# Kernel optimization log

Hardware: AMD Instinct MI355X
Metric: run time of the kernel (lower is better)

Reference implementation:

```python
import jax, jax.numpy as jnp
import numpy as np
import math


def _neighbor_stack(x):
    # x: [b, nc, w, d] -> [b, nc, 3, w, d] with zero-padded prev/next chunks
    prev = jnp.pad(x[:, :-1], ((0, 0), (1, 0), (0, 0), (0, 0)))
    nxt = jnp.pad(x[:, 1:], ((0, 0), (0, 1), (0, 0), (0, 0)))
    return jnp.stack([prev, x, nxt], axis=2)


def local_attention(q, kv, Wq, Wkv, Wo, w):
    b, L, d_model = q.shape
    d_head = Wkv.shape[1] // 2
    h = d_model // d_head
    nc = L // w

    qp = (q @ Wq).reshape(b, L, h, d_head) / math.sqrt(d_head)
    kvp = kv @ Wkv  # [b, L, 2*d_head], single shared KV head (MQA)
    k, v = kvp[..., :d_head], kvp[..., d_head:]

    cq = qp.reshape(b, nc, w, h, d_head)
    k3 = _neighbor_stack(k.reshape(b, nc, w, d_head))  # [b, nc, 3, w, d]
    v3 = _neighbor_stack(v.reshape(b, nc, w, d_head))  # [b, nc, 3, w, d]

    # scores over (prev, self, next) chunks; padded edge chunks contribute
    # zero scores (exp(0)=1 in softmax), exactly as the torch F.pad(value=0) does.
    scores = jnp.einsum('bcxhd,bcpyd->bcxhpy', cq, k3)  # [b,nc,w,h,3,w]
    probs = jax.nn.softmax(scores.reshape(b, nc, w, h, 3 * w), axis=-1)
    probs = probs.reshape(b, nc, w, h, 3, w)

    ctx = jnp.einsum('bcxhpy,bcpyd->bcxhd', probs, v3)  # [b,nc,w,h,d]
    ctx = ctx.reshape(b, L, d_model)
    return ctx @ Wo


def setup_inputs() -> dict:
    key = jax.random.key(0)
    k1, k2, k3, k4, k5 = jax.random.split(key, 5)
    b, L, d_model, n_head = 1, 4096, 1024, 16
    d_head = d_model // n_head
    scale = 0.02
    return {
        'q': jax.random.normal(k1, (b, L, d_model), dtype=jnp.float32),
        'kv': jax.random.normal(k2, (b, L, d_model), dtype=jnp.float32),
        'Wq': jax.random.normal(k3, (d_model, d_model), dtype=jnp.float32) * scale,
        'Wkv': jax.random.normal(k4, (d_model, 2 * d_head), dtype=jnp.float32) * scale,
        'Wo': jax.random.normal(k5, (d_model, d_model), dtype=jnp.float32) * scale,
        'w': 512,
    }


def reference(q, kv, Wq, Wkv, Wo, w):
    return local_attention(q, kv, Wq, Wkv, Wo, w)
```

## Files before the change

kernel.cpp:

```cpp
#include <hip/hip_runtime.h>
#include <hip/hip_bf16.h>

typedef unsigned short u16;
typedef unsigned int u32;
typedef __attribute__((ext_vector_type(8))) short bf16x8;
typedef __attribute__((ext_vector_type(4))) float f32x4;
typedef __attribute__((ext_vector_type(16))) float f32x16;
typedef __attribute__((ext_vector_type(4))) u32 u32x4;

__device__ __forceinline__ u16 f2bf(float x) {
  __hip_bfloat16 h = __float2bfloat16(x);
  return __builtin_bit_cast(u16, h);
}

__device__ __forceinline__ u32 cvtpk(float lo, float hi) {
  u32 d;
  asm("v_cvt_pk_bf16_f32 %0, %1, %2" : "=v"(d) : "v"(lo), "v"(hi));
  return d;
}

#if __has_builtin(__builtin_amdgcn_exp2f)
#define EXP2(x) __builtin_amdgcn_exp2f(x)
#else
#define EXP2(x) __expf((x) * 0.6931471805599453f)
#endif

__device__ __forceinline__ bf16x8 mk_frag(u32 a, u32 b, u32 c, u32 d) {
  u32x4 v = {a, b, c, d};
  return __builtin_bit_cast(bf16x8, v);
}

__device__ __forceinline__ f32x16 mfma32(bf16x8 a, bf16x8 b, f32x16 c) {
  return __builtin_amdgcn_mfma_f32_32x32x16_bf16(a, b, c, 0, 0, 0);
}

__device__ __forceinline__ void gload16(const void* g, void* lds) {
  __builtin_amdgcn_global_load_lds((const __attribute__((address_space(1))) void*)g,
                                   (__attribute__((address_space(3))) void*)lds, 16, 0, 0);
}

__global__ __launch_bounds__(256) void cvt_tw(const float* __restrict__ q, const float* __restrict__ kv,
                                              const float* __restrict__ Wq, const float* __restrict__ Wkv,
                                              const float* __restrict__ Wo, u16* __restrict__ qkbf,
                                              u16* __restrict__ wqt, u16* __restrict__ wkvt,
                                              u16* __restrict__ wot) {
  __shared__ float T[64][65];
  const int t = threadIdx.x;
  const int bid = blockIdx.x;
  if (bid < 4096) {
    int idx = bid * 256 + t;
    const float* src = (idx < 524288) ? q : kv;
    int li = idx & 524287;
    const float4* p = (const float4*)src + (size_t)li * 2;
    float4 a = p[0], b = p[1];
    bf16x8 vv;
    vv[0] = (short)f2bf(a.x); vv[1] = (short)f2bf(a.y);
    vv[2] = (short)f2bf(a.z); vv[3] = (short)f2bf(a.w);
    vv[4] = (short)f2bf(b.x); vv[5] = (short)f2bf(b.y);
    vv[6] = (short)f2bf(b.z); vv[7] = (short)f2bf(b.w);
    *(bf16x8*)(qkbf + (size_t)idx * 8) = vv;
    return;
  }
  const int wb = bid - 4096;
  const float* W; u16* Wt; int N, bx, by;
  if (wb < 256)      { W = Wq;  Wt = wqt;  N = 1024; bx = wb & 15; by = wb >> 4; }
  else if (wb < 512) { int b = wb - 256; W = Wo;  Wt = wot;  N = 1024; bx = b & 15; by = b >> 4; }
  else               { int b = wb - 512; W = Wkv; Wt = wkvt; N = 128;  bx = b & 1;  by = b >> 1; }
  const int K = 1024;
  const int n0 = bx * 64, k0 = by * 64;
  #pragma unroll
  for (int pass = 0; pass < 4; ++pass) {
    int r = pass * 16 + (t >> 4);
    int c = (t & 15) * 4;
    float4 v = *(const float4*)(W + (size_t)(k0 + r) * N + n0 + c);
    T[r][c] = v.x; T[r][c + 1] = v.y; T[r][c + 2] = v.z; T[r][c + 3] = v.w;
  }
  __syncthreads();
  #pragma unroll
  for (int s = 0; s < 2; ++s) {
    int n = s * 32 + (t >> 3);
    int kk = (t & 7) * 8;
    bf16x8 vv;
    #pragma unroll
    for (int i = 0; i < 8; ++i) vv[i] = (short)f2bf(T[kk + i][n]);
    *(bf16x8*)(Wt + (size_t)(n0 + n) * K + k0 + kk) = vv;
  }
}

template<int BF16OUT>
__global__ __launch_bounds__(256, 3) void gemm_bt(const u16* __restrict__ A, const u16* __restrict__ Bt,
                                                  void* __restrict__ Cout, int N, int K, float scale) {
  __shared__ __attribute__((aligned(16))) u16 As[128 * 128];
  __shared__ __attribute__((aligned(16))) u16 Bs[64 * 128];
  const int t = threadIdx.x;
  const int lane = t & 63, wv = t >> 6;
  const int g = lane >> 4, i16 = lane & 15;
  const int m0 = blockIdx.y * 128, n0 = blockIdx.x * 64;
  const int wr = wv >> 1, wc = wv & 1;
  f32x4 acc[4][2] = {};
  for (int kt = 0; kt < K; kt += 128) {
    #pragma unroll
    for (int j = 0; j < 8; ++j) {
      int p = j * 4096 + t * 16;
      int row = p >> 8;
      int lg = (p & 255) ^ ((row & 15) << 4);
      gload16(A + (size_t)(m0 + row) * K + kt + (lg >> 1), (char*)As + p);
    }
    #pragma unroll
    for (int j = 0; j < 4; ++j) {
      int p = j * 4096 + t * 16;
      int row = p >> 8;
      int lg = (p & 255) ^ ((row & 15) << 4);
      gload16(Bt + (size_t)(n0 + row) * K + kt + (lg >> 1), (char*)Bs + p);
    }
    __syncthreads();
    bf16x8 af[4][4], bfr[4][2];
    #pragma unroll
    for (int kf = 0; kf < 4; ++kf) {
      #pragma unroll
      for (int x = 0; x < 4; ++x) {
        int ra = wr * 64 + x * 16 + i16;
        af[kf][x] = *(const bf16x8*)((const char*)As + ((ra * 256 + kf * 64 + g * 16) ^ ((ra & 15) << 4)));
      }
      #pragma unroll
      for (int x = 0; x < 2; ++x) {
        int rb = wc * 32 + x * 16 + i16;
        bfr[kf][x] = *(const bf16x8*)((const char*)Bs + ((rb * 256 + kf * 64 + g * 16) ^ ((rb & 15) << 4)));
      }
    }
    #pragma unroll
    for (int kf = 0; kf < 4; ++kf)
      #pragma unroll
      for (int mi = 0; mi < 4; ++mi)
        #pragma unroll
        for (int ni = 0; ni < 2; ++ni)
          acc[mi][ni] = __builtin_amdgcn_mfma_f32_16x16x32_bf16(af[kf][mi], bfr[kf][ni], acc[mi][ni], 0, 0, 0);
    __syncthreads();
  }
  #pragma unroll
  for (int mi = 0; mi < 4; ++mi)
    #pragma unroll
    for (int ni = 0; ni < 2; ++ni)
      #pragma unroll
      for (int r = 0; r < 4; ++r) {
        size_t off = (size_t)(m0 + wr * 64 + mi * 16 + g * 4 + r) * N + (n0 + wc * 32 + ni * 16 + i16);
        float v = acc[mi][ni][r] * scale;
        if (BF16OUT) ((u16*)Cout)[off] = f2bf(v);
        else ((float*)Cout)[off] = v;
      }
}

__global__ __launch_bounds__(256, 3) void gemm_qkv(const u16* __restrict__ qbf, const u16* __restrict__ kvbf,
                                                   const u16* __restrict__ wqt, const u16* __restrict__ wkvt,
                                                   u16* __restrict__ qp, u16* __restrict__ kvp,
                                                   u16* __restrict__ vtg) {
  __shared__ __attribute__((aligned(16))) u16 As[128 * 128];
  __shared__ __attribute__((aligned(16))) u16 Bs[64 * 128];
  const int t = threadIdx.x;
  const int lane = t & 63, wv = t >> 6;
  const int g = lane >> 4, i16 = lane & 15;
  const int wr = wv >> 1, wc = wv & 1;
  const int K = 1024;
  const int bid = blockIdx.x;
  const bool iskv = bid >= 512;
  const u16* A; const u16* Bt; int m0, n0;
  if (!iskv) { A = qbf;  Bt = wqt;  m0 = (bid >> 4) * 128; n0 = (bid & 15) * 64; }
  else       { int b = bid - 512; A = kvbf; Bt = wkvt; m0 = (b >> 1) * 128; n0 = (b & 1) * 64; }
  f32x4 acc[4][2] = {};
  for (int kt = 0; kt < K; kt += 128) {
    #pragma unroll
    for (int j = 0; j < 8; ++j) {
      int p = j * 4096 + t * 16;
      int row = p >> 8;
      int lg = (p & 255) ^ ((row & 15) << 4);
      gload16(A + (size_t)(m0 + row) * K + kt + (lg >> 1), (char*)As + p);
    }
    #pragma unroll
    for (int j = 0; j < 4; ++j) {
      int p = j * 4096 + t * 16;
      int row = p >> 8;
      int lg = (p & 255) ^ ((row & 15) << 4);
      gload16(Bt + (size_t)(n0 + row) * K + kt + (lg >> 1), (char*)Bs + p);
    }
    __syncthreads();
    bf16x8 af[4][4], bfr[4][2];
    #pragma unroll
    for (int kf = 0; kf < 4; ++kf) {
      #pragma unroll
      for (int x = 0; x < 4; ++x) {
        int ra = wr * 64 + x * 16 + i16;
        af[kf][x] = *(const bf16x8*)((const char*)As + ((ra * 256 + kf * 64 + g * 16) ^ ((ra & 15) << 4)));
      }
      #pragma unroll
      for (int x = 0; x < 2; ++x) {
        int rb = wc * 32 + x * 16 + i16;
        bfr[kf][x] = *(const bf16x8*)((const char*)Bs + ((rb * 256 + kf * 64 + g * 16) ^ ((rb & 15) << 4)));
      }
    }
    #pragma unroll
    for (int kf = 0; kf < 4; ++kf)
      #pragma unroll
      for (int mi = 0; mi < 4; ++mi)
        #pragma unroll
        for (int ni = 0; ni < 2; ++ni)
          acc[mi][ni] = __builtin_amdgcn_mfma_f32_16x16x32_bf16(af[kf][mi], bfr[kf][ni], acc[mi][ni], 0, 0, 0);
    __syncthreads();
  }
  if (!iskv) {
    #pragma unroll
    for (int mi = 0; mi < 4; ++mi)
      #pragma unroll
      for (int ni = 0; ni < 2; ++ni)
        #pragma unroll
        for (int r = 0; r < 4; ++r)
          qp[(size_t)(m0 + wr * 64 + mi * 16 + g * 4 + r) * 1024 + n0 + wc * 32 + ni * 16 + i16] =
              f2bf(acc[mi][ni][r] * 0.18033688011112042f);
  } else if (n0 == 0) {
    #pragma unroll
    for (int mi = 0; mi < 4; ++mi)
      #pragma unroll
      for (int ni = 0; ni < 2; ++ni)
        #pragma unroll
        for (int r = 0; r < 4; ++r)
          kvp[(size_t)(m0 + wr * 64 + mi * 16 + g * 4 + r) * 64 + wc * 32 + ni * 16 + i16] =
              f2bf(acc[mi][ni][r]);
  } else {
    u16* CT = (u16*)As;
    #pragma unroll
    for (int mi = 0; mi < 4; ++mi)
      #pragma unroll
      for (int ni = 0; ni < 2; ++ni)
        #pragma unroll
        for (int r = 0; r < 4; ++r)
          CT[(wc * 32 + ni * 16 + i16) * 128 + wr * 64 + mi * 16 + g * 4 + r] = f2bf(acc[mi][ni][r]);
    __syncthreads();
    int d = t >> 2, c4 = t & 3;
    const u16* src = CT + d * 128 + c4 * 32;
    u16* dst = vtg + (size_t)d * 4096 + m0 + c4 * 32;
    #pragma unroll
    for (int j = 0; j < 4; ++j)
      *(bf16x8*)(dst + j * 8) = *(const bf16x8*)(src + j * 8);
  }
}

__global__ __launch_bounds__(256, 2) void attn_kernel(const u16* __restrict__ qp, const u16* __restrict__ kvp,
                                                      const u16* __restrict__ vtg, u16* __restrict__ ctx) {
  __shared__ __attribute__((aligned(16))) u16 Ks[2][2][64 * 64];
  __shared__ __attribute__((aligned(16))) u16 Vs[2][2][64 * 64];
  const int t = threadIdx.x;
  const int lane = t & 63, wv = t >> 6;
  const int g2 = wv >> 1, wq = wv & 1;
  const int tg = t & 127;
  const int hh = lane >> 5, q32 = lane & 31;
  const int bid = blockIdx.x;
  const int qt = bid & 3, hd = (bid >> 2) & 15, c = bid >> 6;
  const int q0 = c * 512 + qt * 128 + wq * 64;
  const int pk32 = (q32 & 19) | ((q32 & 4) << 1) | ((q32 & 8) >> 1);

  bf16x8 qfA[4], qfB[4];
  #pragma unroll
  for (int dt = 0; dt < 4; ++dt) {
    qfA[dt] = *(const bf16x8*)(qp + (size_t)(q0 + q32) * 1024 + hd * 64 + dt * 16 + hh * 8);
    qfB[dt] = *(const bf16x8*)(qp + (size_t)(q0 + 32 + q32) * 1024 + hd * 64 + dt * 16 + hh * 8);
  }

  const int kb0 = (c - 1) * 512;
  const int v0 = (c == 0) ? 8 : 0;
  const int nv = (c == 0 || c == 7) ? 16 : 24;
  const int n2 = nv >> 1;
  const int s0 = v0 + g2 * n2;
  const float lpad = g2 ? 0.f : 32.f * (float)(24 - nv);
  float lA = lpad, lB = lpad;
  f32x16 accA[2] = {}, accB[2] = {};

  int kA[4], vA[4];
  #pragma unroll
  for (int j = 0; j < 4; ++j) {
    int p = j * 2048 + tg * 16;
    int row = p >> 7;
    int lg = (p & 127) ^ ((row & 7) << 4);
    kA[j] = row * 64 + (lg >> 1);
    vA[j] = row * 4096 + (lg >> 1);
  }

  auto stage = [&](int b, int tile) {
    const int kb = kb0 + tile * 64;
    #pragma unroll
    for (int j = 0; j < 4; ++j)
      gload16(kvp + (size_t)(kb * 64 + kA[j]), (char*)Ks[g2][b] + j * 2048 + tg * 16);
    #pragma unroll
    for (int j = 0; j < 4; ++j)
      gload16(vtg + (size_t)(kb + vA[j]), (char*)Vs[g2][b] + j * 2048 + tg * 16);
  };

  stage(0, s0);

  for (int i = 0; i < n2; ++i) {
    asm volatile("s_waitcnt vmcnt(0)" ::: "memory");
    __builtin_amdgcn_s_barrier();
    if (i + 1 < n2) stage((i + 1) & 1, s0 + i + 1);
    const char* kbase0 = (const char*)Ks[g2][i & 1];
    const char* vbase0 = (const char*)Vs[g2][i & 1];
    f32x16 sA[2] = {}, sB[2] = {};
    #pragma unroll
    for (int kt = 0; kt < 2; ++kt) {
      const char* kbase = kbase0 + kt * 4096 + pk32 * 128;
      int kswz = (pk32 & 7) << 4;
      #pragma unroll
      for (int dt = 0; dt < 4; ++dt) {
        bf16x8 kf = *(const bf16x8*)(kbase + ((dt * 32 + hh * 16) ^ kswz));
        sA[kt] = mfma32(kf, qfA[dt], sA[kt]);
        sB[kt] = mfma32(kf, qfB[dt], sB[kt]);
      }
    }
    #pragma unroll
    for (int kt = 0; kt < 2; ++kt) {
      #pragma unroll
      for (int r = 0; r < 16; ++r) sA[kt][r] = EXP2(sA[kt][r]);
      #pragma unroll
      for (int r = 0; r < 16; ++r) sB[kt][r] = EXP2(sB[kt][r]);
      lA += (((sA[kt][0] + sA[kt][1]) + (sA[kt][2] + sA[kt][3])) + ((sA[kt][4] + sA[kt][5]) + (sA[kt][6] + sA[kt][7]))) +
            (((sA[kt][8] + sA[kt][9]) + (sA[kt][10] + sA[kt][11])) + ((sA[kt][12] + sA[kt][13]) + (sA[kt][14] + sA[kt][15])));
      lB += (((sB[kt][0] + sB[kt][1]) + (sB[kt][2] + sB[kt][3])) + ((sB[kt][4] + sB[kt][5]) + (sB[kt][6] + sB[kt][7]))) +
            (((sB[kt][8] + sB[kt][9]) + (sB[kt][10] + sB[kt][11])) + ((sB[kt][12] + sB[kt][13]) + (sB[kt][14] + sB[kt][15])));
      u32 wA[8], wB[8];
      #pragma unroll
      for (int j = 0; j < 8; ++j) wA[j] = cvtpk(sA[kt][2 * j], sA[kt][2 * j + 1]);
      #pragma unroll
      for (int j = 0; j < 8; ++j) wB[j] = cvtpk(sB[kt][2 * j], sB[kt][2 * j + 1]);
      bf16x8 pbA0 = mk_frag(wA[0], wA[1], wA[2], wA[3]);
      bf16x8 pbA1 = mk_frag(wA[4], wA[5], wA[6], wA[7]);
      bf16x8 pbB0 = mk_frag(wB[0], wB[1], wB[2], wB[3]);
      bf16x8 pbB1 = mk_frag(wB[4], wB[5], wB[6], wB[7]);
      int vswz = (q32 & 7) << 4;
      #pragma unroll
      for (int dtv = 0; dtv < 2; ++dtv) {
        const char* vbase = vbase0 + dtv * 4096 + q32 * 128;
        bf16x8 va0 = *(const bf16x8*)(vbase + ((kt * 64 + hh * 16) ^ vswz));
        accA[dtv] = mfma32(va0, pbA0, accA[dtv]);
        accB[dtv] = mfma32(va0, pbB0, accB[dtv]);
        bf16x8 va1 = *(const bf16x8*)(vbase + ((kt * 64 + 32 + hh * 16) ^ vswz));
        accA[dtv] = mfma32(va1, pbA1, accA[dtv]);
        accB[dtv] = mfma32(va1, pbB1, accB[dtv]);
      }
    }
  }

  __syncthreads();
  char* M = (char*)&Ks[0][0][0];
  float* Lx = (float*)((char*)&Vs[0][0][0] + 24576);
  if (g2 == 1) {
    #pragma unroll
    for (int set = 0; set < 2; ++set) {
      const f32x16* ac = set ? accB : accA;
      #pragma unroll
      for (int dtv = 0; dtv < 2; ++dtv)
        #pragma unroll
        for (int j = 0; j < 4; ++j) {
          f32x4 chunk = {ac[dtv][4 * j], ac[dtv][4 * j + 1], ac[dtv][4 * j + 2], ac[dtv][4 * j + 3]};
          int byte = lane * 128 + dtv * 64 + j * 16;
          *(f32x4*)(M + wq * 16384 + set * 8192 + (byte ^ ((lane & 7) << 4))) = chunk;
        }
      Lx[(wq * 2 + set) * 64 + lane] = set ? lB : lA;
    }
  }
  __syncthreads();
  if (g2 == 0) {
    #pragma unroll
    for (int set = 0; set < 2; ++set) {
      f32x16* ac = set ? accB : accA;
      #pragma unroll
      for (int dtv = 0; dtv < 2; ++dtv)
        #pragma unroll
        for (int j = 0; j < 4; ++j) {
          int byte = lane * 128 + dtv * 64 + j * 16;
          f32x4 chunk = *(const f32x4*)(M + wq * 16384 + set * 8192 + (byte ^ ((lane & 7) << 4)));
          #pragma unroll
          for (int e = 0; e < 4; ++e) ac[dtv][4 * j + e] += chunk[e];
        }
      float l = (set ? lB : lA) + Lx[(wq * 2 + set) * 64 + lane];
      l += __shfl_xor(l, 32);
      float rl = 1.0f / l;
      char* Ow = (char*)&Vs[0][0][0] + wq * 4096;
      #pragma unroll
      for (int dtv = 0; dtv < 2; ++dtv)
        #pragma unroll
        for (int j = 0; j < 4; ++j) {
          int d = dtv * 32 + 8 * j + 4 * hh;
          uint2 wp;
          wp.x = cvtpk(ac[dtv][4 * j] * rl, ac[dtv][4 * j + 1] * rl);
          wp.y = cvtpk(ac[dtv][4 * j + 2] * rl, ac[dtv][4 * j + 3] * rl);
          *(uint2*)(Ow + q32 * 128 + ((d * 2) ^ ((q32 & 7) << 4))) = wp;
        }
      asm volatile("s_waitcnt lgkmcnt(0)" ::: "memory");
      __builtin_amdgcn_sched_barrier(0);
      #pragma unroll
      for (int rep = 0; rep < 4; ++rep) {
        int q = lane >> 1, dblk = (lane & 1) * 4 + rep, d0 = dblk * 8;
        bf16x8 ov = *(const bf16x8*)(Ow + q * 128 + ((d0 * 2) ^ ((q & 7) << 4)));
        *(bf16x8*)(ctx + (size_t)(q0 + set * 32 + q) * 1024 + hd * 64 + d0) = ov;
      }
      asm volatile("s_waitcnt lgkmcnt(0) vmcnt(0)" ::: "memory");
      __builtin_amdgcn_sched_barrier(0);
    }
  }
}

extern "C" void kernel_launch(void* const* d_in, const int* in_sizes, int n_in,
                              void* d_out, int out_size, void* d_ws, size_t ws_size,
                              hipStream_t stream) {
  const float* q   = (const float*)d_in[0];
  const float* kv  = (const float*)d_in[1];
  const float* Wq  = (const float*)d_in[2];
  const float* Wkv = (const float*)d_in[3];
  const float* Wo  = (const float*)d_in[4];
  char* ws = (char*)d_ws;
  u16* qbf  = (u16*)(ws);
  u16* ctx  = (u16*)(ws);
  u16* kvbf = (u16*)(ws + 8388608);
  u16* qp   = (u16*)(ws + 16777216);
  u16* kvp  = (u16*)(ws + 25165824);
  u16* vtg  = (u16*)(ws + 25690112);
  u16* wqt  = (u16*)(ws + 26214400);
  u16* wkvt = (u16*)(ws + 28311552);
  u16* wot  = (u16*)(ws + 28573696);
  cvt_tw<<<4640, 256, 0, stream>>>(q, kv, Wq, Wkv, Wo, qbf, wqt, wkvt, wot);
  gemm_qkv<<<576, 256, 0, stream>>>(qbf, kvbf, wqt, wkvt, qp, kvp, vtg);
  attn_kernel<<<512, 256, 0, stream>>>(qp, kvp, vtg, ctx);
  gemm_bt<0><<<dim3(16, 32), 256, 0, stream>>>(ctx, wot, (float*)d_out, 1024, 1024, 1.0f);
}
```

Measured before the change: 84.07 us.

## Load K/V MFMA fragments directly from global memory, dropping LDS staging

The attention loop no longer stages K and V tiles into double-buffered shared memory with per-iteration barriers. Each lane now loads its K and V MFMA fragments straight from global memory into registers, and the loop is unrolled by two. Shared memory shrinks to a single buffer that is only used for the final cross-wave reduction and the output transpose. This removes barrier and LDS traffic, but every wave now issues its own uncoalesced 16-byte global loads with no explicit prefetch, and register pressure goes up.

After: 101.6 us. 20.9% more time.

```diff
diff --git a/kernel.cpp b/kernel.cpp
--- a/kernel.cpp
+++ b/kernel.cpp
@@ -245,12 +245,10 @@
 
 __global__ __launch_bounds__(256, 2) void attn_kernel(const u16* __restrict__ qp, const u16* __restrict__ kvp,
                                                       const u16* __restrict__ vtg, u16* __restrict__ ctx) {
-  __shared__ __attribute__((aligned(16))) u16 Ks[2][2][64 * 64];
-  __shared__ __attribute__((aligned(16))) u16 Vs[2][2][64 * 64];
+  __shared__ __attribute__((aligned(16))) char MLDS[43008];
   const int t = threadIdx.x;
   const int lane = t & 63, wv = t >> 6;
   const int g2 = wv >> 1, wq = wv & 1;
-  const int tg = t & 127;
   const int hh = lane >> 5, q32 = lane & 31;
   const int bid = blockIdx.x;
   const int qt = bid & 3, hd = (bid >> 2) & 15, c = bid >> 6;
@@ -268,50 +266,37 @@
   const int v0 = (c == 0) ? 8 : 0;
   const int nv = (c == 0 || c == 7) ? 16 : 24;
   const int n2 = nv >> 1;
-  const int s0 = v0 + g2 * n2;
+  const int kbs = kb0 + (v0 + g2 * n2) * 64;
   const float lpad = g2 ? 0.f : 32.f * (float)(24 - nv);
   float lA = lpad, lB = lpad;
   f32x16 accA[2] = {}, accB[2] = {};
 
-  int kA[4], vA[4];
-  #pragma unroll
-  for (int j = 0; j < 4; ++j) {
-    int p = j * 2048 + tg * 16;
-    int row = p >> 7;
-    int lg = (p & 127) ^ ((row & 7) << 4);
-    kA[j] = row * 64 + (lg >> 1);
-    vA[j] = row * 4096 + (lg >> 1);
-  }
-
-  auto stage = [&](int b, int tile) {
-    const int kb = kb0 + tile * 64;
-    #pragma unroll
-    for (int j = 0; j < 4; ++j)
-      gload16(kvp + (size_t)(kb * 64 + kA[j]), (char*)Ks[g2][b] + j * 2048 + tg * 16);
-    #pragma unroll
-    for (int j = 0; j < 4; ++j)
-      gload16(vtg + (size_t)(kb + vA[j]), (char*)Vs[g2][b] + j * 2048 + tg * 16);
-  };
-
-  stage(0, s0);
-
+  const u16* kp0 = kvp + (size_t)(kbs + pk32) * 64 + hh * 8;
+  const u16* kp1 = kvp + (size_t)(kbs + 32 + pk32) * 64 + hh * 8;
+  const u16* vp0 = vtg + (size_t)q32 * 4096 + kbs + hh * 8;
+  const u16* vp1 = vtg + (size_t)(32 + q32) * 4096 + kbs + hh * 8;
+
+  #pragma unroll 2
   for (int i = 0; i < n2; ++i) {
-    asm volatile("s_waitcnt vmcnt(0)" ::: "memory");
-    __builtin_amdgcn_s_barrier();
-    if (i + 1 < n2) stage((i + 1) & 1, s0 + i + 1);
-    const char* kbase0 = (const char*)Ks[g2][i & 1];
-    const char* vbase0 = (const char*)Vs[g2][i & 1];
+    bf16x8 kf0[4], kf1[4];
+    #pragma unroll
+    for (int dt = 0; dt < 4; ++dt) {
+      kf0[dt] = *(const bf16x8*)(kp0 + dt * 16);
+      kf1[dt] = *(const bf16x8*)(kp1 + dt * 16);
+    }
+    bf16x8 va[2][4];
+    #pragma unroll
+    for (int kj = 0; kj < 4; ++kj) {
+      va[0][kj] = *(const bf16x8*)(vp0 + kj * 16);
+      va[1][kj] = *(const bf16x8*)(vp1 + kj * 16);
+    }
     f32x16 sA[2] = {}, sB[2] = {};
     #pragma unroll
-    for (int kt = 0; kt < 2; ++kt) {
-      const char* kbase = kbase0 + kt * 4096 + pk32 * 128;
-      int kswz = (pk32 & 7) << 4;
-      #pragma unroll
-      for (int dt = 0; dt < 4; ++dt) {
-        bf16x8 kf = *(const bf16x8*)(kbase + ((dt * 32 + hh * 16) ^ kswz));
-        sA[kt] = mfma32(kf, qfA[dt], sA[kt]);
-        sB[kt] = mfma32(kf, qfB[dt], sB[kt]);
-      }
+    for (int dt = 0; dt < 4; ++dt) {
+      sA[0] = mfma32(kf0[dt], qfA[dt], sA[0]);
+      sB[0] = mfma32(kf0[dt], qfB[dt], sB[0]);
+      sA[1] = mfma32(kf1[dt], qfA[dt], sA[1]);
+      sB[1] = mfma32(kf1[dt], qfB[dt], sB[1]);
     }
     #pragma unroll
     for (int kt = 0; kt < 2; ++kt) {
@@ -332,23 +317,20 @@
       bf16x8 pbA1 = mk_frag(wA[4], wA[5], wA[6], wA[7]);
       bf16x8 pbB0 = mk_frag(wB[0], wB[1], wB[2], wB[3]);
       bf16x8 pbB1 = mk_frag(wB[4], wB[5], wB[6], wB[7]);
-      int vswz = (q32 & 7) << 4;
       #pragma unroll
       for (int dtv = 0; dtv < 2; ++dtv) {
-        const char* vbase = vbase0 + dtv * 4096 + q32 * 128;
-        bf16x8 va0 = *(const bf16x8*)(vbase + ((kt * 64 + hh * 16) ^ vswz));
-        accA[dtv] = mfma32(va0, pbA0, accA[dtv]);
-        accB[dtv] = mfma32(va0, pbB0, accB[dtv]);
-        bf16x8 va1 = *(const bf16x8*)(vbase + ((kt * 64 + 32 + hh * 16) ^ vswz));
-        accA[dtv] = mfma32(va1, pbA1, accA[dtv]);
-        accB[dtv] = mfma32(va1, pbB1, accB[dtv]);
-      }
-    }
-  }
-
+        accA[dtv] = mfma32(va[dtv][kt * 2], pbA0, accA[dtv]);
+        accB[dtv] = mfma32(va[dtv][kt * 2], pbB0, accB[dtv]);
+        accA[dtv] = mfma32(va[dtv][kt * 2 + 1], pbA1, accA[dtv]);
+        accB[dtv] = mfma32(va[dtv][kt * 2 + 1], pbB1, accB[dtv]);
+      }
+    }
+    kp0 += 4096; kp1 += 4096; vp0 += 64; vp1 += 64;
+  }
+
+  char* M = MLDS;
+  float* Lx = (float*)(MLDS + 32768);
   __syncthreads();
-  char* M = (char*)&Ks[0][0][0];
-  float* Lx = (float*)((char*)&Vs[0][0][0] + 24576);
   if (g2 == 1) {
     #pragma unroll
     for (int set = 0; set < 2; ++set) {
@@ -381,7 +363,7 @@
       float l = (set ? lB : lA) + Lx[(wq * 2 + set) * 64 + lane];
       l += __shfl_xor(l, 32);
       float rl = 1.0f / l;
-      char* Ow = (char*)&Vs[0][0][0] + wq * 4096;
+      char* Ow = MLDS + 34816 + wq * 4096;
       #pragma unroll
       for (int dtv = 0; dtv < 2; ++dtv)
         #pragma unroll
```
